# Performance work log

Measured on AMD Instinct MI355X. Metric: run time of the kernel, lower is better.

Reference implementation:

```python
import jax, jax.numpy as jnp
import numpy as np

B, W, R, D = 2, 4096, 8, 32


def setup_inputs() -> dict:
    key = jax.random.key(0)
    k1, k2, k3 = jax.random.split(key, 3)
    q_alpha = jax.random.normal(k1, (B, W, R), dtype=jnp.float32)
    k = jax.random.normal(k2, (B, W, R), dtype=jnp.float32)
    h_norm = jax.random.normal(k3, (B, W, D), dtype=jnp.float32)
    # RetNet-style decay rates per rank channel: gamma_i = 1 - 2^{-(6+i)} in (0, 1)
    gamma_vec = 1.0 - jnp.exp2(-(6.0 + jnp.arange(R, dtype=jnp.float32)))
    idx = jnp.arange(W)
    decay_diff = (idx[:, None] - idx[None, :]).astype(jnp.float32)  # [W, W], i - j
    causal_mask = (idx[:, None] >= idx[None, :]).astype(jnp.float32)  # [W, W] lower-tri
    return {
        "q_alpha": q_alpha,
        "k": k,
        "h_norm": h_norm,
        "gamma_vec": gamma_vec,
        "causal_mask": causal_mask,
        "decay_diff": decay_diff,
    }


def reference(q_alpha, k, h_norm, gamma_vec, causal_mask, decay_diff):
    # q_alpha, k: [B, W, R]; h_norm: [B, W, D]; gamma_vec: [R]; masks: [W, W]
    window = h_norm.shape[1]
    kh = k[..., :, None] * h_norm[..., None, :]  # [B, W, R, D]
    dist = decay_diff[:window, :window][..., None]  # [W, W, 1]
    log_gamma = jnp.log(jnp.clip(gamma_vec, 1e-8, None)).reshape(1, 1, -1)  # [1, 1, R]
    causal = causal_mask[:window, :window][..., None]  # [W, W, 1]
    decay_mask = jnp.exp(dist * log_gamma) * causal  # [W, W, R]
    causal_inner = jnp.einsum("ijr,bjrd->bird", decay_mask, kh)  # [B, W, R, D]
    return jnp.einsum("bwr,bwrd->bwd", q_alpha, causal_inner)  # [B, W, D]
```

## Files before the change

kernel.cpp:

```cpp
#include <hip/hip_runtime.h>

#define B 2
#define W 4096
#define R 8
#define D 32
#define L 64
#define C (W / L)

__device__ __forceinline__ float gpow6(float g, int e) {
    float p = 1.f;
    float b = g;
#pragma unroll
    for (int bit = 0; bit < 6; ++bit) {
        p = (e & (1 << bit)) ? p * b : p;
        b *= b;
    }
    return p;
}

__global__ __launch_bounds__(512) void k_local(const float* __restrict__ kin,
                                               const float* __restrict__ hin,
                                               const float* __restrict__ gamma_vec,
                                               float* __restrict__ ws_state) {
    __shared__ float sk[L][R];
    __shared__ float sh[L][D];
    __shared__ float part[2][R][D];
    const int blk = blockIdx.x;
    const int b = blk / C, c = blk % C;
    const int t = threadIdx.x;
    const float* kp = kin + ((size_t)b * W + (size_t)c * L) * R;
    const float* hp = hin + ((size_t)b * W + (size_t)c * L) * D;
    ((float*)sk)[t] = kp[t];
    ((float4*)sh)[t] = ((const float4*)hp)[t];
    __syncthreads();
    const int half = t >> 8;
    const int rd = t & 255;
    const int r = rd >> 5, d = rd & 31;
    const float g = gamma_vec[r];
    const float g2 = g * g;
    float S = 0.f;
#pragma unroll
    for (int m = 0; m < 32; ++m) {
        const int j = 2 * m + half;
        S = S * g2 + sk[j][r] * sh[j][d];
    }
    part[half][r][d] = S;
    __syncthreads();
    if (t < 256) {
        ws_state[(size_t)(b * C + c) * R * D + rd] = part[1][r][d] + g * part[0][r][d];
    }
}

__global__ __launch_bounds__(512) void k_out(const float* __restrict__ qin,
                                             const float* __restrict__ kin,
                                             const float* __restrict__ hin,
                                             const float* __restrict__ gamma_vec,
                                             const float* __restrict__ ws_state,
                                             float* __restrict__ out) {
    __shared__ float sqg[R][L];
    __shared__ float skg[R][L];
    __shared__ float sh[L][D];
    __shared__ __align__(16) float sAT[L][L + 4];
    __shared__ float s0[R][D];
    const int blk = blockIdx.x;
    const int b = blk / C, c = blk % C;
    const int t = threadIdx.x;
    const size_t row0 = (size_t)b * W + (size_t)c * L;

    if (t >= 256) {
        const int u = t - 256;
        const float* hp = hin + row0 * D;
        ((float4*)sh)[u]       = ((const float4*)hp)[u];
        ((float4*)sh)[u + 256] = ((const float4*)hp)[u + 256];
        const int i = (u & 127) >> 1;
        const int r0 = (u & 1) * 4;
        if (u < 128) {
            const float4 v = ((const float4*)(qin + row0 * R))[u];
            sqg[r0 + 0][i] = v.x * gpow6(gamma_vec[r0 + 0], i);
            sqg[r0 + 1][i] = v.y * gpow6(gamma_vec[r0 + 1], i);
            sqg[r0 + 2][i] = v.z * gpow6(gamma_vec[r0 + 2], i);
            sqg[r0 + 3][i] = v.w * gpow6(gamma_vec[r0 + 3], i);
        } else {
            const float4 v = ((const float4*)(kin + row0 * R))[u - 128];
            skg[r0 + 0][i] = v.x * gpow6(1.f / gamma_vec[r0 + 0], i);
            skg[r0 + 1][i] = v.y * gpow6(1.f / gamma_vec[r0 + 1], i);
            skg[r0 + 2][i] = v.z * gpow6(1.f / gamma_vec[r0 + 2], i);
            skg[r0 + 3][i] = v.w * gpow6(1.f / gamma_vec[r0 + 3], i);
        }
    } else {
        const int r = t >> 5;
        const float g = gamma_vec[r];
        float gL = g;
#pragma unroll
        for (int s = 0; s < 6; ++s) gL *= gL;
        float gp[9];
        gp[0] = 1.f;
#pragma unroll
        for (int e = 1; e <= 8; ++e) gp[e] = gp[e - 1] * gL;
        float P = 0.f;
        const float* wsp = ws_state + (size_t)b * C * R * D + t;
        int cc = 0;
        const int head = c & 7;
        for (; cc < head; ++cc) P = P * gL + wsp[(size_t)cc * 256];
        for (; cc < c; cc += 8) {
            const float v0 = wsp[(size_t)(cc + 0) * 256];
            const float v1 = wsp[(size_t)(cc + 1) * 256];
            const float v2 = wsp[(size_t)(cc + 2) * 256];
            const float v3 = wsp[(size_t)(cc + 3) * 256];
            const float v4 = wsp[(size_t)(cc + 4) * 256];
            const float v5 = wsp[(size_t)(cc + 5) * 256];
            const float v6 = wsp[(size_t)(cc + 6) * 256];
            const float v7 = wsp[(size_t)(cc + 7) * 256];
            const float sg = v0 * gp[7] + v1 * gp[6] + v2 * gp[5] + v3 * gp[4]
                           + v4 * gp[3] + v5 * gp[2] + v6 * gp[1] + v7;
            P = P * gp[8] + sg;
        }
        s0[r][t & 31] = g * P;
    }
    __syncthreads();

    const int i = t & 63;
    const int w = t >> 6;
    float qreg[R];
#pragma unroll
    for (int r = 0; r < R; ++r) qreg[r] = sqg[r][i];
#pragma unroll
    for (int p = 0; p < 8; ++p) {
        const int j = w + 8 * p;
        float a = 0.f;
#pragma unroll
        for (int r = 0; r < R; ++r) a += qreg[r] * skg[r][j];
        sAT[j][i] = (j <= i) ? a : 0.f;
    }
    __syncthreads();

    const int d = t & 31;
    const int ig = t >> 5;
    float pr[R];
#pragma unroll
    for (int r = 0; r < R; ++r) pr[r] = s0[r][d];
    float acc[4];
#pragma unroll
    for (int s = 0; s < 4; ++s) {
        const int i2 = ig * 4 + s;
        float a = 0.f;
#pragma unroll
        for (int r = 0; r < R; ++r) a += sqg[r][i2] * pr[r];
        acc[s] = a;
    }
    const int jmax = ig * 4 + 3;
    for (int j = 0; j <= jmax; ++j) {
        const float hv = sh[j][d];
        const float4 av = *(const float4*)&sAT[j][ig * 4];
        acc[0] += av.x * hv; acc[1] += av.y * hv;
        acc[2] += av.z * hv; acc[3] += av.w * hv;
    }
#pragma unroll
    for (int s = 0; s < 4; ++s)
        out[(row0 + (size_t)(ig * 4 + s)) * D + d] = acc[s];
}

extern "C" void kernel_launch(void* const* d_in, const int* in_sizes, int n_in,
                              void* d_out, int out_size, void* d_ws, size_t ws_size,
                              hipStream_t stream) {
    const float* q  = (const float*)d_in[0];
    const float* k  = (const float*)d_in[1];
    const float* h  = (const float*)d_in[2];
    const float* gv = (const float*)d_in[3];
    float* out = (float*)d_out;
    float* ws  = (float*)d_ws;

    k_local<<<B * C, 512, 0, stream>>>(k, h, gv, ws);
    k_out  <<<B * C, 512, 0, stream>>>(q, k, h, gv, ws, out);
}
```

Before: 135.7 us.

## Fuse chunk-state and output kernels with a grid-wide atomic barrier

Merges the local chunk-state kernel and the output kernel into one launch. The blocks synchronise through a global atomic counter, which is reset by a memset before each launch. Each block also preloads all prior chunk states with a fully unrolled predicated scan, and overlaps the carry-in computation (threads 0-255) with the intra-chunk attention matrix build (threads 256-511). This is meant to remove a kernel launch and the gap between kernels, but it relies on all 128 blocks being co-resident and adds a memset plus spin-waiting.

Result: slower. 152.2 us (+12.2%).

```diff
diff --git a/kernel.cpp b/kernel.cpp
--- a/kernel.cpp
+++ b/kernel.cpp
@@ -6,6 +6,7 @@
 #define D 32
 #define L 64
 #define C (W / L)
+#define NBLK (B * C)
 
 __device__ __forceinline__ float gpow6(float g, int e) {
     float p = 1.f;
@@ -18,119 +19,108 @@
     return p;
 }
 
-__global__ __launch_bounds__(512) void k_local(const float* __restrict__ kin,
+__global__ __launch_bounds__(512) void k_fused(const float* __restrict__ qin,
+                                               const float* __restrict__ kin,
                                                const float* __restrict__ hin,
                                                const float* __restrict__ gamma_vec,
-                                               float* __restrict__ ws_state) {
-    __shared__ float sk[L][R];
-    __shared__ float sh[L][D];
-    __shared__ float part[2][R][D];
-    const int blk = blockIdx.x;
-    const int b = blk / C, c = blk % C;
-    const int t = threadIdx.x;
-    const float* kp = kin + ((size_t)b * W + (size_t)c * L) * R;
-    const float* hp = hin + ((size_t)b * W + (size_t)c * L) * D;
-    ((float*)sk)[t] = kp[t];
-    ((float4*)sh)[t] = ((const float4*)hp)[t];
-    __syncthreads();
-    const int half = t >> 8;
-    const int rd = t & 255;
-    const int r = rd >> 5, d = rd & 31;
-    const float g = gamma_vec[r];
-    const float g2 = g * g;
-    float S = 0.f;
-#pragma unroll
-    for (int m = 0; m < 32; ++m) {
-        const int j = 2 * m + half;
-        S = S * g2 + sk[j][r] * sh[j][d];
-    }
-    part[half][r][d] = S;
-    __syncthreads();
-    if (t < 256) {
-        ws_state[(size_t)(b * C + c) * R * D + rd] = part[1][r][d] + g * part[0][r][d];
-    }
-}
-
-__global__ __launch_bounds__(512) void k_out(const float* __restrict__ qin,
-                                             const float* __restrict__ kin,
-                                             const float* __restrict__ hin,
-                                             const float* __restrict__ gamma_vec,
-                                             const float* __restrict__ ws_state,
-                                             float* __restrict__ out) {
+                                               float* __restrict__ ws_state,
+                                               unsigned int* __restrict__ counter,
+                                               float* __restrict__ out) {
     __shared__ float sqg[R][L];
     __shared__ float skg[R][L];
+    __shared__ float sk[L][R];
     __shared__ float sh[L][D];
     __shared__ __align__(16) float sAT[L][L + 4];
     __shared__ float s0[R][D];
+    __shared__ float part[2][R][D];
     const int blk = blockIdx.x;
     const int b = blk / C, c = blk % C;
     const int t = threadIdx.x;
     const size_t row0 = (size_t)b * W + (size_t)c * L;
 
-    if (t >= 256) {
-        const int u = t - 256;
-        const float* hp = hin + row0 * D;
-        ((float4*)sh)[u]       = ((const float4*)hp)[u];
-        ((float4*)sh)[u + 256] = ((const float4*)hp)[u + 256];
-        const int i = (u & 127) >> 1;
-        const int r0 = (u & 1) * 4;
-        if (u < 128) {
-            const float4 v = ((const float4*)(qin + row0 * R))[u];
-            sqg[r0 + 0][i] = v.x * gpow6(gamma_vec[r0 + 0], i);
-            sqg[r0 + 1][i] = v.y * gpow6(gamma_vec[r0 + 1], i);
-            sqg[r0 + 2][i] = v.z * gpow6(gamma_vec[r0 + 2], i);
-            sqg[r0 + 3][i] = v.w * gpow6(gamma_vec[r0 + 3], i);
-        } else {
-            const float4 v = ((const float4*)(kin + row0 * R))[u - 128];
-            skg[r0 + 0][i] = v.x * gpow6(1.f / gamma_vec[r0 + 0], i);
-            skg[r0 + 1][i] = v.y * gpow6(1.f / gamma_vec[r0 + 1], i);
-            skg[r0 + 2][i] = v.z * gpow6(1.f / gamma_vec[r0 + 2], i);
-            skg[r0 + 3][i] = v.w * gpow6(1.f / gamma_vec[r0 + 3], i);
+    ((float4*)sh)[t] = ((const float4*)(hin + row0 * D))[t];
+    if (t < 128) {
+        const int i = t >> 1, r0 = (t & 1) * 4;
+        const float4 v = ((const float4*)(qin + row0 * R))[t];
+        sqg[r0 + 0][i] = v.x * gpow6(gamma_vec[r0 + 0], i);
+        sqg[r0 + 1][i] = v.y * gpow6(gamma_vec[r0 + 1], i);
+        sqg[r0 + 2][i] = v.z * gpow6(gamma_vec[r0 + 2], i);
+        sqg[r0 + 3][i] = v.w * gpow6(gamma_vec[r0 + 3], i);
+    } else if (t < 256) {
+        const int u = t - 128;
+        const int i = u >> 1, r0 = (u & 1) * 4;
+        const float4 v = ((const float4*)(kin + row0 * R))[u];
+        sk[i][r0 + 0] = v.x; sk[i][r0 + 1] = v.y;
+        sk[i][r0 + 2] = v.z; sk[i][r0 + 3] = v.w;
+        skg[r0 + 0][i] = v.x * gpow6(1.f / gamma_vec[r0 + 0], i);
+        skg[r0 + 1][i] = v.y * gpow6(1.f / gamma_vec[r0 + 1], i);
+        skg[r0 + 2][i] = v.z * gpow6(1.f / gamma_vec[r0 + 2], i);
+        skg[r0 + 3][i] = v.w * gpow6(1.f / gamma_vec[r0 + 3], i);
+    }
+    __syncthreads();
+
+    {
+        const int half = t >> 8;
+        const int rd = t & 255;
+        const int r = rd >> 5, d = rd & 31;
+        const float g = gamma_vec[r];
+        const float g2 = g * g;
+        float S = 0.f;
+#pragma unroll
+        for (int m = 0; m < 32; ++m) {
+            const int j = 2 * m + half;
+            S = S * g2 + sk[j][r] * sh[j][d];
         }
-    } else {
+        part[half][r][d] = S;
+        __syncthreads();
+        if (t < 256) {
+            const float val = part[1][r][d] + g * part[0][r][d];
+            __hip_atomic_store(&ws_state[(size_t)blk * 256 + rd], val,
+                               __ATOMIC_RELAXED, __HIP_MEMORY_SCOPE_AGENT);
+        }
+    }
+    __threadfence();
+    __syncthreads();
+
+    if (t == 0) {
+        atomicAdd(counter, 1u);
+        while (__hip_atomic_load(counter, __ATOMIC_ACQUIRE,
+                                 __HIP_MEMORY_SCOPE_AGENT) < NBLK) {}
+    }
+    __syncthreads();
+
+    if (t < 256) {
         const int r = t >> 5;
         const float g = gamma_vec[r];
         float gL = g;
 #pragma unroll
         for (int s = 0; s < 6; ++s) gL *= gL;
-        float gp[9];
-        gp[0] = 1.f;
+        float* wsp = ws_state + (size_t)b * C * 256 + t;
+        float v[C - 1];
 #pragma unroll
-        for (int e = 1; e <= 8; ++e) gp[e] = gp[e - 1] * gL;
+        for (int cc = 0; cc < C - 1; ++cc)
+            v[cc] = __hip_atomic_load(wsp + (size_t)cc * 256,
+                                      __ATOMIC_RELAXED, __HIP_MEMORY_SCOPE_AGENT);
         float P = 0.f;
-        const float* wsp = ws_state + (size_t)b * C * R * D + t;
-        int cc = 0;
-        const int head = c & 7;
-        for (; cc < head; ++cc) P = P * gL + wsp[(size_t)cc * 256];
-        for (; cc < c; cc += 8) {
-            const float v0 = wsp[(size_t)(cc + 0) * 256];
-            const float v1 = wsp[(size_t)(cc + 1) * 256];
-            const float v2 = wsp[(size_t)(cc + 2) * 256];
-            const float v3 = wsp[(size_t)(cc + 3) * 256];
-            const float v4 = wsp[(size_t)(cc + 4) * 256];
-            const float v5 = wsp[(size_t)(cc + 5) * 256];
-            const float v6 = wsp[(size_t)(cc + 6) * 256];
-            const float v7 = wsp[(size_t)(cc + 7) * 256];
-            const float sg = v0 * gp[7] + v1 * gp[6] + v2 * gp[5] + v3 * gp[4]
-                           + v4 * gp[3] + v5 * gp[2] + v6 * gp[1] + v7;
-            P = P * gp[8] + sg;
+#pragma unroll
+        for (int cc = 0; cc < C - 1; ++cc)
+            P = (cc < c) ? P * gL + v[cc] : P;
+        s0[r][t & 31] = g * P;
+    } else {
+        const int u = t - 256;
+        const int i = u & 63;
+        const int w2 = u >> 6;
+        float qreg[R];
+#pragma unroll
+        for (int r = 0; r < R; ++r) qreg[r] = sqg[r][i];
+#pragma unroll
+        for (int p = 0; p < 16; ++p) {
+            const int j = w2 + 4 * p;
+            float a = 0.f;
+#pragma unroll
+            for (int r = 0; r < R; ++r) a += qreg[r] * skg[r][j];
+            sAT[j][i] = (j <= i) ? a : 0.f;
         }
-        s0[r][t & 31] = g * P;
-    }
-    __syncthreads();
-
-    const int i = t & 63;
-    const int w = t >> 6;
-    float qreg[R];
-#pragma unroll
-    for (int r = 0; r < R; ++r) qreg[r] = sqg[r][i];
-#pragma unroll
-    for (int p = 0; p < 8; ++p) {
-        const int j = w + 8 * p;
-        float a = 0.f;
-#pragma unroll
-        for (int r = 0; r < R; ++r) a += qreg[r] * skg[r][j];
-        sAT[j][i] = (j <= i) ? a : 0.f;
     }
     __syncthreads();
 
@@ -170,6 +160,7 @@
     float* out = (float*)d_out;
     float* ws  = (float*)d_ws;
 
-    k_local<<<B * C, 512, 0, stream>>>(k, h, gv, ws);
-    k_out  <<<B * C, 512, 0, stream>>>(q, k, h, gv, ws, out);
+    unsigned int* counter = (unsigned int*)((char*)d_ws + 128 * 1024);
+    hipMemsetAsync(counter, 0, sizeof(unsigned int), stream);
+    k_fused<<<NBLK, 512, 0, stream>>>(q, k, h, gv, ws, counter, out);
 }
```

## Prefetch all chunk states unconditionally and overlap prefix scan with intra-chunk matrix

Applied to the files above, without the earlier changes.

The first 256 threads now issue all 63 workspace state loads up front into a register array, with fixed trip counts and no dependence on c, instead of a data-dependent unrolled loop. The prefix recurrence then runs as a predicated fully unrolled loop, and the other 256 threads build the masked intra-chunk attention matrix at the same time, with the two halves split across a new barrier. The aim is to hide global load latency and overlap the serial scan with the matrix build. In exchange every block loads all states regardless of its chunk index, and the 63-float register array raises register pressure and may lower occupancy.

Result: no change. 133.8 us (-1.4%).

```diff
diff --git a/kernel.cpp b/kernel.cpp
--- a/kernel.cpp
+++ b/kernel.cpp
@@ -67,7 +67,13 @@
     const int t = threadIdx.x;
     const size_t row0 = (size_t)b * W + (size_t)c * L;
 
-    if (t >= 256) {
+    float v[C - 1];
+    if (t < 256) {
+        const float* wsp = ws_state + (size_t)b * C * 256 + t;
+#pragma unroll
+        for (int cc = 0; cc < C - 1; ++cc)
+            v[cc] = wsp[(size_t)cc * 256];
+    } else {
         const int u = t - 256;
         const float* hp = hin + row0 * D;
         ((float4*)sh)[u]       = ((const float4*)hp)[u];
@@ -75,62 +81,47 @@
         const int i = (u & 127) >> 1;
         const int r0 = (u & 1) * 4;
         if (u < 128) {
-            const float4 v = ((const float4*)(qin + row0 * R))[u];
-            sqg[r0 + 0][i] = v.x * gpow6(gamma_vec[r0 + 0], i);
-            sqg[r0 + 1][i] = v.y * gpow6(gamma_vec[r0 + 1], i);
-            sqg[r0 + 2][i] = v.z * gpow6(gamma_vec[r0 + 2], i);
-            sqg[r0 + 3][i] = v.w * gpow6(gamma_vec[r0 + 3], i);
+            const float4 q4 = ((const float4*)(qin + row0 * R))[u];
+            sqg[r0 + 0][i] = q4.x * gpow6(gamma_vec[r0 + 0], i);
+            sqg[r0 + 1][i] = q4.y * gpow6(gamma_vec[r0 + 1], i);
+            sqg[r0 + 2][i] = q4.z * gpow6(gamma_vec[r0 + 2], i);
+            sqg[r0 + 3][i] = q4.w * gpow6(gamma_vec[r0 + 3], i);
         } else {
-            const float4 v = ((const float4*)(kin + row0 * R))[u - 128];
-            skg[r0 + 0][i] = v.x * gpow6(1.f / gamma_vec[r0 + 0], i);
-            skg[r0 + 1][i] = v.y * gpow6(1.f / gamma_vec[r0 + 1], i);
-            skg[r0 + 2][i] = v.z * gpow6(1.f / gamma_vec[r0 + 2], i);
-            skg[r0 + 3][i] = v.w * gpow6(1.f / gamma_vec[r0 + 3], i);
+            const float4 k4 = ((const float4*)(kin + row0 * R))[u - 128];
+            skg[r0 + 0][i] = k4.x * gpow6(1.f / gamma_vec[r0 + 0], i);
+            skg[r0 + 1][i] = k4.y * gpow6(1.f / gamma_vec[r0 + 1], i);
+            skg[r0 + 2][i] = k4.z * gpow6(1.f / gamma_vec[r0 + 2], i);
+            skg[r0 + 3][i] = k4.w * gpow6(1.f / gamma_vec[r0 + 3], i);
         }
-    } else {
+    }
+    __syncthreads();
+
+    if (t < 256) {
         const int r = t >> 5;
         const float g = gamma_vec[r];
         float gL = g;
 #pragma unroll
         for (int s = 0; s < 6; ++s) gL *= gL;
-        float gp[9];
-        gp[0] = 1.f;
+        float P = 0.f;
 #pragma unroll
-        for (int e = 1; e <= 8; ++e) gp[e] = gp[e - 1] * gL;
-        float P = 0.f;
-        const float* wsp = ws_state + (size_t)b * C * R * D + t;
-        int cc = 0;
-        const int head = c & 7;
-        for (; cc < head; ++cc) P = P * gL + wsp[(size_t)cc * 256];
-        for (; cc < c; cc += 8) {
-            const float v0 = wsp[(size_t)(cc + 0) * 256];
-            const float v1 = wsp[(size_t)(cc + 1) * 256];
-            const float v2 = wsp[(size_t)(cc + 2) * 256];
-            const float v3 = wsp[(size_t)(cc + 3) * 256];
-            const float v4 = wsp[(size_t)(cc + 4) * 256];
-            const float v5 = wsp[(size_t)(cc + 5) * 256];
-            const float v6 = wsp[(size_t)(cc + 6) * 256];
-            const float v7 = wsp[(size_t)(cc + 7) * 256];
-            const float sg = v0 * gp[7] + v1 * gp[6] + v2 * gp[5] + v3 * gp[4]
-                           + v4 * gp[3] + v5 * gp[2] + v6 * gp[1] + v7;
-            P = P * gp[8] + sg;
+        for (int cc = 0; cc < C - 1; ++cc)
+            P = (cc < c) ? P * gL + v[cc] : P;
+        s0[r][t & 31] = g * P;
+    } else {
+        const int u = t - 256;
+        const int i = u & 63;
+        const int w2 = u >> 6;
+        float qreg[R];
+#pragma unroll
+        for (int r = 0; r < R; ++r) qreg[r] = sqg[r][i];
+#pragma unroll
+        for (int p = 0; p < 16; ++p) {
+            const int j = w2 + 4 * p;
+            float a = 0.f;
+#pragma unroll
+            for (int r = 0; r < R; ++r) a += qreg[r] * skg[r][j];
+            sAT[j][i] = (j <= i) ? a : 0.f;
         }
-        s0[r][t & 31] = g * P;
-    }
-    __syncthreads();
-
-    const int i = t & 63;
-    const int w = t >> 6;
-    float qreg[R];
-#pragma unroll
-    for (int r = 0; r < R; ++r) qreg[r] = sqg[r][i];
-#pragma unroll
-    for (int p = 0; p < 8; ++p) {
-        const int j = w + 8 * p;
-        float a = 0.f;
-#pragma unroll
-        for (int r = 0; r < R; ++r) a += qreg[r] * skg[r][j];
-        sAT[j][i] = (j <= i) ? a : 0.f;
     }
     __syncthreads();
 
```
